# Kernel tuning notes

Hardware: AMD Instinct MI355X
Metric: run time of the kernel (lower is better)

## Reference

```python
import jax, jax.numpy as jnp
import numpy as np

B, T, H, Dk = 2, 2048, 8, 64
D = H * Dk
MAX_TIMESCALE = 10000.0
MIN_TIMESCALE = 2.0


def sinusoid_position_encoding(seq_len, hidden):
    # Non-causal symmetric relative positions: length 2*seq_len.
    freqs = np.arange(0, hidden, MIN_TIMESCALE)
    inv_freq = MAX_TIMESCALE ** (-freqs / hidden)
    pos_seq = np.arange(seq_len, -seq_len, -1.0)  # [2T]
    sinusoid = np.einsum('i,j->ij', pos_seq, inv_freq)  # [2T, hidden/2]
    pe = np.concatenate([np.sin(sinusoid), np.cos(sinusoid)], axis=-1)
    return jnp.asarray(pe, dtype=jnp.float32)  # [2T, hidden]


def rel_shift(logits):
    # Transformer-XL shift (general, non-causal): [b,h,t,2t] -> [b,h,t,t]
    b, h, t, total = logits.shape  # total == 2t
    x = logits.reshape(b, h, total, t)[:, :, 1:, :]
    x = x.reshape(b, h, t, total - 1)
    return x[..., :t]


def setup_inputs() -> dict:
    key = jax.random.key(0)
    ks = jax.random.split(key, 14)
    s = 1.0 / np.sqrt(D).astype(np.float32)  # VarianceScaling(1.0)-like
    return {
        'query': jax.random.normal(ks[0], (B, T, D), jnp.float32),
        'key_in': jax.random.normal(ks[1], (B, T, D), jnp.float32),
        'value': jax.random.normal(ks[2], (B, T, D), jnp.float32),
        'Wq': jax.random.normal(ks[3], (D, H * Dk), jnp.float32) * s,
        'bq': jnp.zeros((H * Dk,), jnp.float32),
        'Wk': jax.random.normal(ks[4], (D, H * Dk), jnp.float32) * s,
        'bk': jnp.zeros((H * Dk,), jnp.float32),
        'Wv': jax.random.normal(ks[5], (D, H * Dk), jnp.float32) * s,
        'bv': jnp.zeros((H * Dk,), jnp.float32),
        'Wr': jax.random.normal(ks[6], (D, D), jnp.float32) * s,
        'content_bias': jax.random.normal(ks[7], (H, Dk), jnp.float32) * 0.02,
        'relative_bias': jax.random.normal(ks[8], (H, Dk), jnp.float32) * 0.02,
        'Wo': jax.random.normal(ks[9], (H * Dk, D), jnp.float32) * s,
        'bo': jnp.zeros((D,), jnp.float32),
    }


def reference(query, key_in, value, Wq, bq, Wk, bk, Wv, bv, Wr,
              content_bias, relative_bias, Wo, bo):
    q = (query @ Wq + bq).reshape(B, T, H, Dk)
    k = (key_in @ Wk + bk).reshape(B, T, H, Dk)
    v = (value @ Wv + bv).reshape(B, T, H, Dk)

    # Content logits with learned per-head content bias.
    content_logits = jnp.einsum('bthd,bThd->bhtT', q + content_bias, k)

    # Relative-position keys: sinusoid encodings projected (no bias).
    pos = sinusoid_position_encoding(T, D)          # [2T, D]
    rel_k = (pos @ Wr).reshape(2 * T, H, Dk)        # [2T, H, Dk]
    relative_logits = jnp.einsum('bthd,Thd->bhtT', q + relative_bias, rel_k)
    relative_logits = rel_shift(relative_logits)    # [B,H,T,T]

    attn_logits = (content_logits + relative_logits) / np.sqrt(Dk).astype(np.float32)
    attn_weights = jax.nn.softmax(attn_logits)      # [B,H,T,T]

    attn = jnp.einsum('bhtT,bThd->bthd', attn_weights, v)
    attn_vec = attn.reshape(B, T, H * Dk)
    return attn_vec @ Wo + bo
```

## Files before the change

kernel.cpp:

```cpp
#include <hip/hip_runtime.h>
#include <math.h>

#define BB 2
#define TT 2048
#define HH 8
#define DK 64
#define DD 512
#define MM (BB * TT)
#define WSZ (128 * 4096)

typedef unsigned int u32;
typedef unsigned short u16;
typedef __bf16 bf16x8 __attribute__((ext_vector_type(8)));
typedef float f32x4 __attribute__((ext_vector_type(4)));

union frag_u { bf16x8 f; u16 u[8]; u32 w[4]; };

__device__ __forceinline__ void split2(float x, u16& h, u16& l) {
    u32 u = __float_as_uint(x);
    u32 hi = (u + 0x7fffu + ((u >> 16) & 1u)) >> 16;
    float hif = __uint_as_float(hi << 16);
    float lof = x - hif;
    u32 ul = __float_as_uint(lof);
    u32 lo = (ul + 0x7fffu + ((ul >> 16) & 1u)) >> 16;
    h = (u16)hi; l = (u16)lo;
}
__device__ __forceinline__ u16 bf16_rne(float x) {
    u32 u = __float_as_uint(x);
    return (u16)((u + 0x7fffu + ((u >> 16) & 1u)) >> 16);
}

__device__ __forceinline__ void load_lds16(const void* g, void* l) {
    __builtin_amdgcn_global_load_lds(
        (const __attribute__((address_space(1))) void*)g,
        (__attribute__((address_space(3))) void*)l, 16, 0, 0);
}

__device__ __forceinline__ void pack_granule(const float* xs, u16* dt, int g) {
    u32 hw[4], lw[4];
#pragma unroll
    for (int e = 0; e < 4; e++) {
        u16 h0, l0, h1, l1;
        split2(xs[2 * e], h0, l0);
        split2(xs[2 * e + 1], h1, l1);
        hw[e] = (u32)h0 | ((u32)h1 << 16);
        lw[e] = (u32)l0 | ((u32)l1 << 16);
    }
    *(uint4*)(dt + g * 8)        = make_uint4(hw[0], hw[1], hw[2], hw[3]);
    *(uint4*)(dt + 2048 + g * 8) = make_uint4(lw[0], lw[1], lw[2], lw[3]);
}

__global__ __launch_bounds__(256) void prepack_wpe_kernel(
    const float* __restrict__ W0, const float* __restrict__ W1,
    const float* __restrict__ W2, const float* __restrict__ W3,
    const float* __restrict__ W4, u16* __restrict__ dstW,
    u16* __restrict__ dstPe) {
    __shared__ float tw[64][36];
    const int tid = threadIdx.x;
    if (blockIdx.x < 640) {
        const int bid = blockIdx.x;
        const int widx = bid >> 7, loc = bid & 127;
        const int nb2 = loc >> 3, kb = loc & 7;
        const float* Wsrc = widx == 0 ? W0 : widx == 1 ? W1 : widx == 2 ? W2
                          : widx == 3 ? W3 : W4;
        const int kl = tid >> 2, gr = tid & 3;
        const float* p = Wsrc + (size_t)(kb * 64 + kl) * 512 + nb2 * 32 + gr * 8;
        float4 a  = *(const float4*)p;
        float4 b4 = *(const float4*)(p + 4);
        *(float4*)&tw[kl][gr * 8]     = a;
        *(float4*)&tw[kl][gr * 8 + 4] = b4;
        __syncthreads();
        const int n5 = tid >> 3, f = tid & 7, s = f >> 2, kq = f & 3;
        float xs[8];
#pragma unroll
        for (int e = 0; e < 8; e++) xs[e] = tw[s * 32 + kq * 8 + e][n5];
        const int n = n5 & 15, nt = n5 >> 4;
        const int g = nt * 128 + n * 8 + ((4 * s + kq + 5 * n) & 7);
        pack_granule(xs, dstW + (size_t)bid * 4096, g);
    } else {
        const int bid = blockIdx.x - 640;
        const int r = tid >> 3, f = tid & 7;
        const int m  = (bid >> 3) * 32 + r;
        const int c0 = (bid & 7) * 64 + f * 8;
        float xs[8];
#pragma unroll
        for (int e = 0; e < 8; e++) {
            int col = c0 + e;
            int j = col & 255;
            double inv_freq = exp((double)(-2 * j) * (9.210340371976184 / 512.0));
            double ang = (double)(TT - m) * inv_freq;
            xs[e] = (col < 256) ? (float)sin(ang) : (float)cos(ang);
        }
        const int s = f >> 2, kq = f & 3, nt = r >> 4, n = r & 15;
        const int g = nt * 128 + n * 8 + ((4 * s + kq + 5 * n) & 7);
        pack_granule(xs, dstPe + (size_t)bid * 4096, g);
    }
}

__device__ __forceinline__ void prepack_a_body(
    const float* __restrict__ src, u16* __restrict__ dst, int bid, int tid) {
    const int r = tid >> 3, f = tid & 7;
    const float* p = src + ((size_t)(bid >> 3) * 32 + r) * 512
                         + (size_t)(bid & 7) * 64 + f * 8;
    float4 a  = *(const float4*)p;
    float4 b4 = *(const float4*)(p + 4);
    float xs[8] = {a.x, a.y, a.z, a.w, b4.x, b4.y, b4.z, b4.w};
    const int s = f >> 2, kq = f & 3, nt = r >> 4, n = r & 15;
    const int g = nt * 128 + n * 8 + ((4 * s + kq + 5 * n) & 7);
    pack_granule(xs, dst + (size_t)bid * 4096, g);
}

__global__ __launch_bounds__(256) void prepack_a3_kernel(
    const float* __restrict__ sq, const float* __restrict__ sk,
    const float* __restrict__ sv, u16* __restrict__ dq,
    u16* __restrict__ dk, u16* __restrict__ dv) {
    const int sel = blockIdx.x >> 10, sub = blockIdx.x & 1023;
    const float* s = sel == 0 ? sq : sel == 1 ? sk : sv;
    u16* d = sel == 0 ? dq : sel == 1 ? dk : dv;
    prepack_a_body(s, d, sub, threadIdx.x);
}

__device__ __forceinline__ void gemm_full(
    const u16* __restrict__ Apk, const u16* __restrict__ Wpk,
    const float* __restrict__ bias, float* __restrict__ C,
    u16* __restrict__ Ppk, const float* __restrict__ dotv,
    float* __restrict__ dotout, int EPI, int bx, int tid) {
    __shared__ __align__(16) u16 Stage[2][16384];

    const int w = tid >> 6, lane = tid & 63, quad = lane >> 4, c = lane & 15;
    const int mp = bx & 63, nb = bx >> 6;
    const int mq = w >> 1, nq = w & 1;

    auto stage_async = [&](int kb, int half) {
        const u16* s = (w < 2)
            ? Apk + (size_t)((2 * mp + w) * 8 + kb) * 4096
            : Wpk + (size_t)((2 * nb + (w & 1)) * 8 + kb) * 4096;
        const u16* g = s + lane * 8;
        u16* d = Stage[half] + w * 4096;
#pragma unroll
        for (int u2 = 0; u2 < 8; u2++)
            load_lds16(g + u2 * 512, d + u2 * 512);
    };

    stage_async(0, 0);

    f32x4 acc[2][2];
#pragma unroll
    for (int mh = 0; mh < 2; mh++)
#pragma unroll
        for (int nh = 0; nh < 2; nh++) acc[mh][nh] = (f32x4){0.f, 0.f, 0.f, 0.f};

    for (int kb = 0; kb < 8; kb++) {
        const int half = kb & 1;
        __syncthreads();
        if (kb < 7) stage_async(kb + 1, 1 - half);
        const u16* Ab = Stage[half] + mq * 4096;
        const u16* Wb = Stage[half] + 8192 + nq * 4096;
#pragma unroll
        for (int s = 0; s < 2; s++) {
            bf16x8 ah[2], al[2], wh[2], wl[2];
#pragma unroll
            for (int t = 0; t < 2; t++) {
                int g = (t << 7) + (c << 3) + (((s << 2) + quad + 5 * c) & 7);
                ah[t] = *(const bf16x8*)(Ab + g * 8);
                al[t] = *(const bf16x8*)(Ab + 2048 + g * 8);
                wh[t] = *(const bf16x8*)(Wb + g * 8);
                wl[t] = *(const bf16x8*)(Wb + 2048 + g * 8);
            }
#pragma unroll
            for (int mh = 0; mh < 2; mh++)
#pragma unroll
                for (int nh = 0; nh < 2; nh++) {
                    acc[mh][nh] = __builtin_amdgcn_mfma_f32_16x16x32_bf16(
                        ah[mh], wh[nh], acc[mh][nh], 0, 0, 0);
                    acc[mh][nh] = __builtin_amdgcn_mfma_f32_16x16x32_bf16(
                        ah[mh], wl[nh], acc[mh][nh], 0, 0, 0);
                    acc[mh][nh] = __builtin_amdgcn_mfma_f32_16x16x32_bf16(
                        al[mh], wh[nh], acc[mh][nh], 0, 0, 0);
                }
        }
    }

    const int n0 = nb * 64 + nq * 32;
    float bv0 = bias ? bias[n0 + c] : 0.f;
    float bv1 = bias ? bias[n0 + 16 + c] : 0.f;

    if (EPI == 0) {
        const int m0 = mp * 64 + mq * 32;
#pragma unroll
        for (int mh = 0; mh < 2; mh++)
#pragma unroll
            for (int r = 0; r < 4; r++) {
                size_t row = (size_t)(m0 + mh * 16 + quad * 4 + r) * 512;
                C[row + n0 + c]      = acc[mh][0][r] + bv0;
                C[row + n0 + 16 + c] = acc[mh][1][r] + bv1;
            }
        return;
    }

    __syncthreads();
    float (*Cl)[68] = (float (*)[68])Stage;
    {
        const int rbase = mq * 32;
#pragma unroll
        for (int mh = 0; mh < 2; mh++)
#pragma unroll
            for (int r = 0; r < 4; r++) {
                int row = rbase + mh * 16 + quad * 4 + r;
                Cl[row][nq * 32 + c]      = acc[mh][0][r] + bv0;
                Cl[row][nq * 32 + 16 + c] = acc[mh][1][r] + bv1;
            }
    }
    __syncthreads();

    if (EPI == 2) {
        const int b = mp >> 5, jt0 = (mp & 31) * 2;
        const int d = tid >> 2, kq = tid & 3;
        const int n = d & 15;
        const int g = (d >> 4) * 64 + n * 4 + ((kq + (n >> 1)) & 3);
#pragma unroll
        for (int ht = 0; ht < 2; ht++) {
            float xs[8];
#pragma unroll
            for (int e = 0; e < 8; e++) xs[e] = Cl[ht * 32 + kq * 8 + e][d];
            u16* dt = Ppk + (size_t)(b * 512 + nb * 64 + jt0 + ht) * 4096;
            pack_granule(xs, dt, g);
        }
        return;
    }

    {
        const int rr = tid >> 3, f = tid & 7;
        const int s = f >> 2, kq = f & 3, nt = rr >> 4, n = rr & 15;
        const int g = nt * 128 + n * 8 + ((4 * s + kq + 5 * n) & 7);
#pragma unroll
        for (int ht = 0; ht < 2; ht++) {
            float xs[8];
#pragma unroll
            for (int e = 0; e < 8; e++) xs[e] = Cl[ht * 32 + rr][f * 8 + e];
            size_t tidx = (EPI == 1)
                ? (size_t)((mp >> 5) * 512 + nb * 64 + (mp & 31) * 2 + ht)
                : (size_t)(nb * 128 + mp * 2 + ht);
            pack_granule(xs, Ppk + tidx * 4096, g);
        }
    }
    if (tid < 64) {
        const float* dv = dotv + nb * 64;
        const float* rowp = Cl[tid];
        float sacc = 0.f;
#pragma unroll
        for (int d = 0; d < 64; d++) sacc += dv[d] * rowp[d];
        int m = mp * 64 + tid;
        if (EPI == 1) {
            int b = m >> 11, t = m & 2047;
            dotout[((size_t)nb * BB + b) * TT + t] = sacc * 0.125f - 8.0f;
        } else {
            dotout[(size_t)nb * 4096 + m] = sacc * 0.125f;
        }
    }
}

__global__ __launch_bounds__(256, 2) void gemm_mfma_kernel(
    const u16* __restrict__ Apk, const u16* __restrict__ Wpk,
    const float* __restrict__ bias, float* __restrict__ C) {
    gemm_full(Apk, Wpk, bias, C, nullptr, nullptr, nullptr, 0,
              blockIdx.x, threadIdx.x);
}

__global__ __launch_bounds__(256, 2) void gemm_relk_kernel(
    const u16* __restrict__ Apk, const u16* __restrict__ Wpk,
    const float* __restrict__ rb, u16* __restrict__ Rpk,
    float* __restrict__ rbrk) {
    gemm_full(Apk, Wpk, nullptr, nullptr, Rpk, rb, rbrk, 3,
              blockIdx.x, threadIdx.x);
}

__global__ __launch_bounds__(256, 2) void gemm3_mfma_kernel(
    const u16* __restrict__ Aq, const u16* __restrict__ Ak,
    const u16* __restrict__ Av, const u16* __restrict__ Wpk,
    const float* __restrict__ bq, const float* __restrict__ bk,
    const float* __restrict__ bv, const float* __restrict__ cb,
    float* __restrict__ qb, u16* __restrict__ Kpk, u16* __restrict__ Vpk,
    float* __restrict__ cbk) {
    const int widx = blockIdx.x >> 9, bx = blockIdx.x & 511;
    const u16* A = widx == 0 ? Aq : widx == 1 ? Ak : Av;
    const u16* W = Wpk + (size_t)widx * WSZ;
    const float* bias = widx == 0 ? bq : widx == 1 ? bk : bv;
    float* Cq = widx == 0 ? qb : nullptr;
    u16* P = widx == 1 ? Kpk : widx == 2 ? Vpk : nullptr;
    gemm_full(A, W, bias, Cq, P, widx == 1 ? cb : nullptr,
              widx == 1 ? cbk : nullptr, widx, bx, threadIdx.x);
}

__global__ __launch_bounds__(128, 2) void attn_mfma_kernel(
    const float* __restrict__ q, const u16* __restrict__ Kpk,
    const u16* __restrict__ Vpk, const u16* __restrict__ Rpk,
    const float* __restrict__ cbk, const float* __restrict__ rbrk,
    u16* __restrict__ Aout) {
    __shared__ float Ring[2 * 3 * 1120];
    __shared__ __align__(16) u16 Pbuf[2 * 1280];

    const int tid = threadIdx.x;
    const int w = tid >> 6, lane = tid & 63, quad = lane >> 4, c = lane & 15;
    const int bx = blockIdx.x;
    const int h = bx & 7, b = (bx >> 3) & 1, it = bx >> 4;
    const int i0 = it * 32;
    const size_t bh_off = (size_t)b * TT * DD + (size_t)h * DK;

    frag_u qh[2][2], ql[2][2];
#pragma unroll
    for (int rg = 0; rg < 2; rg++) {
        const float* qrow = q + bh_off + (size_t)(i0 + 16 * rg + c) * DD;
#pragma unroll
        for (int s = 0; s < 2; s++) {
            int d0 = s * 32 + quad * 8;
            float4 a  = *(const float4*)(qrow + d0);
            float4 b4 = *(const float4*)(qrow + d0 + 4);
            float xs[8] = {a.x, a.y, a.z, a.w, b4.x, b4.y, b4.z, b4.w};
#pragma unroll
            for (int j2 = 0; j2 < 8; j2++)
                split2(xs[j2] * 0.125f, qh[rg][s].u[j2], ql[rg][s].u[j2]);
        }
    }

    frag_u onesf;
#pragma unroll
    for (int j2 = 0; j2 < 8; j2++) onesf.u[j2] = 0x3f80u;

    const u16* Ktiles  = Kpk + (size_t)(b * HH + h) * 64 * 4096;
    const u16* Vtiles  = Vpk + (size_t)(b * HH + h) * 64 * 4096;
    const u16* Rchunks = Rpk + (size_t)h * 128 * 4096;
    const float* rbrk_h = rbrk + (size_t)h * (2 * TT);
    const float* cbk_h  = cbk + ((size_t)h * BB + b) * TT;

    auto read_kr = [&](const u16* reg, int nt, int s, bf16x8& fh, bf16x8& fl) {
        int g = (nt << 7) + (c << 3) + (((s << 2) + quad + 5 * c) & 7);
        fh = *(const bf16x8*)(reg + g * 8);
        fl = *(const bf16x8*)(reg + 2048 + g * 8);
    };
    auto read_v = [&](const u16* Vb, int ntd, bf16x8& fh, bf16x8& fl) {
        int g = ntd * 64 + c * 4 + ((quad + (c >> 1)) & 3);
        fh = *(const bf16x8*)(Vb + g * 8);
        fl = *(const bf16x8*)(Vb + 2048 + g * 8);
    };

    auto produce = [&](int cidx) {
        const u16* Rc = Rchunks + (size_t)cidx * 4096;
        float* ringw = Ring + (w * 3 + cidx % 3) * 1120;
#pragma unroll
        for (int ntp = 0; ntp < 2; ntp++) {
            f32x4 a0 = {0.f, 0.f, 0.f, 0.f};
            f32x4 a1 = {0.f, 0.f, 0.f, 0.f};
#pragma unroll
            for (int s = 0; s < 2; s++) {
                int g = (ntp << 7) + (c << 3) + (((s << 2) + quad + 5 * c) & 7);
                bf16x8 fh = *(const bf16x8*)(Rc + g * 8);
                bf16x8 fl = *(const bf16x8*)(Rc + 2048 + g * 8);
                a0 = __builtin_amdgcn_mfma_f32_16x16x32_bf16(qh[0][s].f, fh, a0, 0, 0, 0);
                a0 = __builtin_amdgcn_mfma_f32_16x16x32_bf16(qh[0][s].f, fl, a0, 0, 0, 0);
                a0 = __builtin_amdgcn_mfma_f32_16x16x32_bf16(ql[0][s].f, fh, a0, 0, 0, 0);
                a1 = __builtin_amdgcn_mfma_f32_16x16x32_bf16(qh[1][s].f, fh, a1, 0, 0, 0);
                a1 = __builtin_amdgcn_mfma_f32_16x16x32_bf16(qh[1][s].f, fl, a1, 0, 0, 0);
                a1 = __builtin_amdgcn_mfma_f32_16x16x32_bf16(ql[1][s].f, fh, a1, 0, 0, 0);
            }
            float rbv = rbrk_h[cidx * 32 + ntp * 16 + c];
            int mpos = ntp * 16 + c;
#pragma unroll
            for (int r = 0; r < 4; r++)
                ringw[(quad * 4 + r) * 35 + mpos] = a0[r] + rbv;
#pragma unroll
            for (int r = 0; r < 4; r++)
                ringw[(16 + quad * 4 + r) * 35 + mpos] = a1[r] + rbv;
        }
    };

    const int base = TT - i0 + 1024 * w;
    const int F = (base >> 5) - 1;
    produce(F);
    produce(F + 1);

    f32x4 o[2][4];
    f32x4 acc_l[2];
#pragma unroll
    for (int rg = 0; rg < 2; rg++) {
        acc_l[rg] = (f32x4){0.f, 0.f, 0.f, 0.f};
#pragma unroll
        for (int nt = 0; nt < 4; nt++) o[rg][nt] = (f32x4){0.f, 0.f, 0.f, 0.f};
    }

    for (int t = 0; t < 32; t++) {
        const int j0 = 1024 * w + 32 * t;
        const u16* Kb = Ktiles + (size_t)(w * 32 + t) * 4096;
        const u16* Vb = Vtiles + (size_t)(w * 32 + t) * 4096;

        int cnext = F + t + 2;
        if (cnext < 128) produce(cnext);

        const int slo = (F + t) % 3;
        const int shi = (slo == 2) ? 0 : slo + 1;
        const int off_lo = (w * 3 + slo) * 1120;
        const int off_hi = (w * 3 + shi) * 1120;
        float cbv0 = cbk_h[j0 + c];
        float cbv1 = cbk_h[j0 + 16 + c];
        float sv[2][2][4];
#pragma unroll
        for (int nt = 0; nt < 2; nt++) {
            f32x4 sc0 = {0.f, 0.f, 0.f, 0.f};
            f32x4 sc1 = {0.f, 0.f, 0.f, 0.f};
            bf16x8 fh0, fl0, fh1, fl1;
            read_kr(Kb, nt, 0, fh0, fl0);
            read_kr(Kb, nt, 1, fh1, fl1);
            __builtin_amdgcn_s_setprio(1);
            sc0 = __builtin_amdgcn_mfma_f32_16x16x32_bf16(qh[0][0].f, fh0, sc0, 0, 0, 0);
            sc0 = __builtin_amdgcn_mfma_f32_16x16x32_bf16(qh[0][0].f, fl0, sc0, 0, 0, 0);
            sc0 = __builtin_amdgcn_mfma_f32_16x16x32_bf16(ql[0][0].f, fh0, sc0, 0, 0, 0);
            sc0 = __builtin_amdgcn_mfma_f32_16x16x32_bf16(qh[0][1].f, fh1, sc0, 0, 0, 0);
            sc0 = __builtin_amdgcn_mfma_f32_16x16x32_bf16(qh[0][1].f, fl1, sc0, 0, 0, 0);
            sc0 = __builtin_amdgcn_mfma_f32_16x16x32_bf16(ql[0][1].f, fh1, sc0, 0, 0, 0);
            sc1 = __builtin_amdgcn_mfma_f32_16x16x32_bf16(qh[1][0].f, fh0, sc1, 0, 0, 0);
            sc1 = __builtin_amdgcn_mfma_f32_16x16x32_bf16(qh[1][0].f, fl0, sc1, 0, 0, 0);
            sc1 = __builtin_amdgcn_mfma_f32_16x16x32_bf16(ql[1][0].f, fh0, sc1, 0, 0, 0);
            sc1 = __builtin_amdgcn_mfma_f32_16x16x32_bf16(qh[1][1].f, fh1, sc1, 0, 0, 0);
            sc1 = __builtin_amdgcn_mfma_f32_16x16x32_bf16(qh[1][1].f, fl1, sc1, 0, 0, 0);
            sc1 = __builtin_amdgcn_mfma_f32_16x16x32_bf16(ql[1][1].f, fh1, sc1, 0, 0, 0);
            __builtin_amdgcn_s_setprio(0);
            float cbv = nt ? cbv1 : cbv0;
#pragma unroll
            for (int r = 0; r < 4; r++) {
                int row16 = quad * 4 + r;
                int rel0 = nt * 16 + c - row16 + 32;
                float rv0 = Ring[((rel0 >= 32) ? off_hi : off_lo)
                                 + row16 * 35 + (rel0 & 31)];
                sv[0][nt][r] = sc0[r] + rv0 + cbv;
                int rel1 = rel0 - 16;
                float rv1 = Ring[((rel1 >= 32) ? off_hi : off_lo)
                                 + (16 + row16) * 35 + (rel1 & 31)];
                sv[1][nt][r] = sc1[r] + rv1 + cbv;
            }
        }

#pragma unroll
        for (int rg = 0; rg < 2; rg++)
#pragma unroll
            for (int r = 0; r < 4; r++) {
                u16* pb = Pbuf + w * 1280 + (16 * rg + quad * 4 + r) * 40;
                pb[c]      = bf16_rne(__expf(sv[rg][0][r]));
                pb[16 + c] = bf16_rne(__expf(sv[rg][1][r]));
            }

        frag_u ph[2];
#pragma unroll
        for (int rg = 0; rg < 2; rg++) {
            const u16* pb = Pbuf + w * 1280 + (16 * rg + c) * 40 + quad * 8;
            *(uint4*)&ph[rg] = *(const uint4*)pb;
        }
        __builtin_amdgcn_s_setprio(1);
#pragma unroll
        for (int ntd = 0; ntd < 4; ntd++) {
            bf16x8 vh, vl;
            read_v(Vb, ntd, vh, vl);
            o[0][ntd] = __builtin_amdgcn_mfma_f32_16x16x32_bf16(ph[0].f, vh, o[0][ntd], 0, 0, 0);
            o[0][ntd] = __builtin_amdgcn_mfma_f32_16x16x32_bf16(ph[0].f, vl, o[0][ntd], 0, 0, 0);
            o[1][ntd] = __builtin_amdgcn_mfma_f32_16x16x32_bf16(ph[1].f, vh, o[1][ntd], 0, 0, 0);
            o[1][ntd] = __builtin_amdgcn_mfma_f32_16x16x32_bf16(ph[1].f, vl, o[1][ntd], 0, 0, 0);
        }
        acc_l[0] = __builtin_amdgcn_mfma_f32_16x16x32_bf16(ph[0].f, onesf.f, acc_l[0], 0, 0, 0);
        acc_l[1] = __builtin_amdgcn_mfma_f32_16x16x32_bf16(ph[1].f, onesf.f, acc_l[1], 0, 0, 0);
        __builtin_amdgcn_s_setprio(0);
    }

    float* scr = Ring + 3360;
    if (w == 1) {
#pragma unroll
        for (int rg = 0; rg < 2; rg++) {
#pragma unroll
            for (int nt = 0; nt < 4; nt++)
#pragma unroll
                for (int r = 0; r < 4; r++)
                    scr[(16 * rg + quad * 4 + r) * 65 + nt * 16 + c] = o[rg][nt][r];
            if (c == 0) {
#pragma unroll
                for (int r = 0; r < 4; r++)
                    scr[2080 + 16 * rg + quad * 4 + r] = acc_l[rg][r];
            }
        }
    }
    __syncthreads();
    float* Lp = Ring;
    if (w == 0) {
#pragma unroll
        for (int rg = 0; rg < 2; rg++)
#pragma unroll
            for (int r = 0; r < 4; r++) {
                int row16 = quad * 4 + r;
                int row32 = 16 * rg + row16;
                float invl = 1.0f / (acc_l[rg][r] + scr[2080 + row32]);
#pragma unroll
                for (int nt = 0; nt < 4; nt++)
                    Lp[row32 * 68 + nt * 16 + c] =
                        (o[rg][nt][r] + scr[row32 * 65 + nt * 16 + c]) * invl;
            }
    }
    __syncthreads();
    u16* dt = Aout + (size_t)((b * 64 + it) * 8 + h) * 4096;
#pragma unroll
    for (int pass = 0; pass < 2; pass++) {
        int idx = pass * 128 + tid;
        int rr = idx >> 3, f = idx & 7;
        float xs[8];
#pragma unroll
        for (int e = 0; e < 8; e++) xs[e] = Lp[rr * 68 + f * 8 + e];
        int s = f >> 2, kq = f & 3, nt2 = rr >> 4, n = rr & 15;
        int g = nt2 * 128 + n * 8 + ((4 * s + kq + 5 * n) & 7);
        pack_granule(xs, dt, g);
    }
}

extern "C" void kernel_launch(void* const* d_in, const int* in_sizes, int n_in,
                              void* d_out, int out_size, void* d_ws, size_t ws_size,
                              hipStream_t stream) {
    const float* query  = (const float*)d_in[0];
    const float* key_in = (const float*)d_in[1];
    const float* value  = (const float*)d_in[2];
    const float* Wq = (const float*)d_in[3];
    const float* bq = (const float*)d_in[4];
    const float* Wk = (const float*)d_in[5];
    const float* bk = (const float*)d_in[6];
    const float* Wv = (const float*)d_in[7];
    const float* bv = (const float*)d_in[8];
    const float* Wr = (const float*)d_in[9];
    const float* cb = (const float*)d_in[10];
    const float* rb = (const float*)d_in[11];
    const float* Wo = (const float*)d_in[12];
    const float* bo = (const float*)d_in[13];
    float* out = (float*)d_out;

    float* ws = (float*)d_ws;
    const size_t SL = (size_t)MM * DD;
    float* qb   = ws;
    u16*   Kpk  = (u16*)(ws + 1 * SL);
    u16*   Vpk  = (u16*)(ws + 2 * SL);
    u16*   Rpk  = (u16*)(ws + 3 * SL);
    u16*   s4   = (u16*)(ws + 4 * SL);
    u16*   s5   = (u16*)(ws + 5 * SL);
    u16*   s6   = (u16*)(ws + 6 * SL);
    u16*   Wpk  = (u16*)(ws + 7 * SL);
    float* cbk  = ws + 7 * SL + 1310720;
    float* rbrk = cbk + BB * TT * HH;

    prepack_wpe_kernel<<<1664, 256, 0, stream>>>(Wq, Wk, Wv, Wr, Wo, Wpk, s6);

    gemm_relk_kernel<<<512, 256, 0, stream>>>(s6, Wpk + 3 * WSZ, rb, Rpk, rbrk);

    prepack_a3_kernel<<<3072, 256, 0, stream>>>(query, key_in, value,
                                                s6, s5, s4);
    gemm3_mfma_kernel<<<1536, 256, 0, stream>>>(s6, s5, s4, Wpk, bq, bk, bv,
                                                cb, qb, Kpk, Vpk, cbk);

    attn_mfma_kernel<<<BB * HH * (TT / 32), 128, 0, stream>>>(
        qb, Kpk, Vpk, Rpk, cbk, rbrk, s4);

    gemm_mfma_kernel<<<512, 256, 0, stream>>>(s4, Wpk + 4 * WSZ, bo, out);
}
```

Measured before the change: 250.5 us.

## Software-pipeline K fragment loads and hoist R/V loads in attention loop

Restructures the attention inner loop into a two-stage unrolled body that double-buffers K fragments in registers, loading the next tile's K while the current tile's QK MFMAs run. R-chunk and V fragments are issued as global loads at the top of each iteration, and the relative-logit ring production is moved after the score computation so that memory latency overlaps with MFMA work. This adds substantial register pressure, which risks lower occupancy or spills.

After: 399.6 us. 1.6x slower.

```diff
diff --git a/kernel.cpp b/kernel.cpp
--- a/kernel.cpp
+++ b/kernel.cpp
@@ -376,6 +376,18 @@
 
     const int base = TT - i0 + 1024 * w;
     const int F = (base >> 5) - 1;
+
+    bf16x8 KAh[2][2], KAl[2][2], KBh[2][2], KBl[2][2];
+    auto load_Kfr = [&](int tile, bf16x8 (&fh)[2][2], bf16x8 (&fl)[2][2]) {
+        const u16* Kb = Ktiles + (size_t)tile * 4096;
+#pragma unroll
+        for (int nt = 0; nt < 2; nt++)
+#pragma unroll
+            for (int s = 0; s < 2; s++)
+                read_kr(Kb, nt, s, fh[nt][s], fl[nt][s]);
+    };
+
+    load_Kfr(w * 32, KAh, KAl);
     produce(F);
     produce(F + 1);
 
@@ -388,42 +400,60 @@
         for (int nt = 0; nt < 4; nt++) o[rg][nt] = (f32x4){0.f, 0.f, 0.f, 0.f};
     }
 
-    for (int t = 0; t < 32; t++) {
+    auto body = [&](int t, bf16x8 (&ckh)[2][2], bf16x8 (&ckl)[2][2],
+                    bf16x8 (&nkh)[2][2], bf16x8 (&nkl)[2][2]) {
         const int j0 = 1024 * w + 32 * t;
-        const u16* Kb = Ktiles + (size_t)(w * 32 + t) * 4096;
-        const u16* Vb = Vtiles + (size_t)(w * 32 + t) * 4096;
-
-        int cnext = F + t + 2;
-        if (cnext < 128) produce(cnext);
+        const int cnext = F + t + 2;
+
+        bf16x8 rfh[2][2], rfl[2][2];
+        if (cnext < 128) {
+            const u16* Rc = Rchunks + (size_t)cnext * 4096;
+#pragma unroll
+            for (int ntp = 0; ntp < 2; ntp++)
+#pragma unroll
+                for (int s = 0; s < 2; s++) {
+                    int g = (ntp << 7) + (c << 3) + (((s << 2) + quad + 5 * c) & 7);
+                    rfh[ntp][s] = *(const bf16x8*)(Rc + g * 8);
+                    rfl[ntp][s] = *(const bf16x8*)(Rc + 2048 + g * 8);
+                }
+        }
+        bf16x8 vfh[4], vfl[4];
+        {
+            const u16* Vb = Vtiles + (size_t)(w * 32 + t) * 4096;
+#pragma unroll
+            for (int ntd = 0; ntd < 4; ntd++) read_v(Vb, ntd, vfh[ntd], vfl[ntd]);
+        }
+        float cbv0 = cbk_h[j0 + c];
+        float cbv1 = cbk_h[j0 + 16 + c];
+
+        f32x4 sc0[2], sc1[2];
+        __builtin_amdgcn_s_setprio(1);
+#pragma unroll
+        for (int nt = 0; nt < 2; nt++) {
+            f32x4 a0 = {0.f, 0.f, 0.f, 0.f};
+            f32x4 a1 = {0.f, 0.f, 0.f, 0.f};
+#pragma unroll
+            for (int s = 0; s < 2; s++) {
+                a0 = __builtin_amdgcn_mfma_f32_16x16x32_bf16(qh[0][s].f, ckh[nt][s], a0, 0, 0, 0);
+                a0 = __builtin_amdgcn_mfma_f32_16x16x32_bf16(qh[0][s].f, ckl[nt][s], a0, 0, 0, 0);
+                a0 = __builtin_amdgcn_mfma_f32_16x16x32_bf16(ql[0][s].f, ckh[nt][s], a0, 0, 0, 0);
+                a1 = __builtin_amdgcn_mfma_f32_16x16x32_bf16(qh[1][s].f, ckh[nt][s], a1, 0, 0, 0);
+                a1 = __builtin_amdgcn_mfma_f32_16x16x32_bf16(qh[1][s].f, ckl[nt][s], a1, 0, 0, 0);
+                a1 = __builtin_amdgcn_mfma_f32_16x16x32_bf16(ql[1][s].f, ckh[nt][s], a1, 0, 0, 0);
+            }
+            sc0[nt] = a0; sc1[nt] = a1;
+        }
+        __builtin_amdgcn_s_setprio(0);
+
+        if (t < 31) load_Kfr(w * 32 + t + 1, nkh, nkl);
 
         const int slo = (F + t) % 3;
         const int shi = (slo == 2) ? 0 : slo + 1;
         const int off_lo = (w * 3 + slo) * 1120;
         const int off_hi = (w * 3 + shi) * 1120;
-        float cbv0 = cbk_h[j0 + c];
-        float cbv1 = cbk_h[j0 + 16 + c];
         float sv[2][2][4];
 #pragma unroll
         for (int nt = 0; nt < 2; nt++) {
-            f32x4 sc0 = {0.f, 0.f, 0.f, 0.f};
-            f32x4 sc1 = {0.f, 0.f, 0.f, 0.f};
-            bf16x8 fh0, fl0, fh1, fl1;
-            read_kr(Kb, nt, 0, fh0, fl0);
-            read_kr(Kb, nt, 1, fh1, fl1);
-            __builtin_amdgcn_s_setprio(1);
-            sc0 = __builtin_amdgcn_mfma_f32_16x16x32_bf16(qh[0][0].f, fh0, sc0, 0, 0, 0);
-            sc0 = __builtin_amdgcn_mfma_f32_16x16x32_bf16(qh[0][0].f, fl0, sc0, 0, 0, 0);
-            sc0 = __builtin_amdgcn_mfma_f32_16x16x32_bf16(ql[0][0].f, fh0, sc0, 0, 0, 0);
-            sc0 = __builtin_amdgcn_mfma_f32_16x16x32_bf16(qh[0][1].f, fh1, sc0, 0, 0, 0);
-            sc0 = __builtin_amdgcn_mfma_f32_16x16x32_bf16(qh[0][1].f, fl1, sc0, 0, 0, 0);
-            sc0 = __builtin_amdgcn_mfma_f32_16x16x32_bf16(ql[0][1].f, fh1, sc0, 0, 0, 0);
-            sc1 = __builtin_amdgcn_mfma_f32_16x16x32_bf16(qh[1][0].f, fh0, sc1, 0, 0, 0);
-            sc1 = __builtin_amdgcn_mfma_f32_16x16x32_bf16(qh[1][0].f, fl0, sc1, 0, 0, 0);
-            sc1 = __builtin_amdgcn_mfma_f32_16x16x32_bf16(ql[1][0].f, fh0, sc1, 0, 0, 0);
-            sc1 = __builtin_amdgcn_mfma_f32_16x16x32_bf16(qh[1][1].f, fh1, sc1, 0, 0, 0);
-            sc1 = __builtin_amdgcn_mfma_f32_16x16x32_bf16(qh[1][1].f, fl1, sc1, 0, 0, 0);
-            sc1 = __builtin_amdgcn_mfma_f32_16x16x32_bf16(ql[1][1].f, fh1, sc1, 0, 0, 0);
-            __builtin_amdgcn_s_setprio(0);
             float cbv = nt ? cbv1 : cbv0;
 #pragma unroll
             for (int r = 0; r < 4; r++) {
@@ -431,12 +461,40 @@
                 int rel0 = nt * 16 + c - row16 + 32;
                 float rv0 = Ring[((rel0 >= 32) ? off_hi : off_lo)
                                  + row16 * 35 + (rel0 & 31)];
-                sv[0][nt][r] = sc0[r] + rv0 + cbv;
+                sv[0][nt][r] = sc0[nt][r] + rv0 + cbv;
                 int rel1 = rel0 - 16;
                 float rv1 = Ring[((rel1 >= 32) ? off_hi : off_lo)
                                  + (16 + row16) * 35 + (rel1 & 31)];
-                sv[1][nt][r] = sc1[r] + rv1 + cbv;
-            }
+                sv[1][nt][r] = sc1[nt][r] + rv1 + cbv;
+            }
+        }
+
+        if (cnext < 128) {
+            float* ringw = Ring + (w * 3 + cnext % 3) * 1120;
+            __builtin_amdgcn_s_setprio(1);
+#pragma unroll
+            for (int ntp = 0; ntp < 2; ntp++) {
+                f32x4 a0 = {0.f, 0.f, 0.f, 0.f};
+                f32x4 a1 = {0.f, 0.f, 0.f, 0.f};
+#pragma unroll
+                for (int s = 0; s < 2; s++) {
+                    a0 = __builtin_amdgcn_mfma_f32_16x16x32_bf16(qh[0][s].f, rfh[ntp][s], a0, 0, 0, 0);
+                    a0 = __builtin_amdgcn_mfma_f32_16x16x32_bf16(qh[0][s].f, rfl[ntp][s], a0, 0, 0, 0);
+                    a0 = __builtin_amdgcn_mfma_f32_16x16x32_bf16(ql[0][s].f, rfh[ntp][s], a0, 0, 0, 0);
+                    a1 = __builtin_amdgcn_mfma_f32_16x16x32_bf16(qh[1][s].f, rfh[ntp][s], a1, 0, 0, 0);
+                    a1 = __builtin_amdgcn_mfma_f32_16x16x32_bf16(qh[1][s].f, rfl[ntp][s], a1, 0, 0, 0);
+                    a1 = __builtin_amdgcn_mfma_f32_16x16x32_bf16(ql[1][s].f, rfh[ntp][s], a1, 0, 0, 0);
+                }
+                float rbv = rbrk_h[cnext * 32 + ntp * 16 + c];
+                int mpos = ntp * 16 + c;
+#pragma unroll
+                for (int r = 0; r < 4; r++)
+                    ringw[(quad * 4 + r) * 35 + mpos] = a0[r] + rbv;
+#pragma unroll
+                for (int r = 0; r < 4; r++)
+                    ringw[(16 + quad * 4 + r) * 35 + mpos] = a1[r] + rbv;
+            }
+            __builtin_amdgcn_s_setprio(0);
         }
 
 #pragma unroll
@@ -447,26 +505,29 @@
                 pb[c]      = bf16_rne(__expf(sv[rg][0][r]));
                 pb[16 + c] = bf16_rne(__expf(sv[rg][1][r]));
             }
-
         frag_u ph[2];
 #pragma unroll
         for (int rg = 0; rg < 2; rg++) {
             const u16* pb = Pbuf + w * 1280 + (16 * rg + c) * 40 + quad * 8;
             *(uint4*)&ph[rg] = *(const uint4*)pb;
         }
+
         __builtin_amdgcn_s_setprio(1);
 #pragma unroll
         for (int ntd = 0; ntd < 4; ntd++) {
-            bf16x8 vh, vl;
-            read_v(Vb, ntd, vh, vl);
-            o[0][ntd] = __builtin_amdgcn_mfma_f32_16x16x32_bf16(ph[0].f, vh, o[0][ntd], 0, 0, 0);
-            o[0][ntd] = __builtin_amdgcn_mfma_f32_16x16x32_bf16(ph[0].f, vl, o[0][ntd], 0, 0, 0);
-            o[1][ntd] = __builtin_amdgcn_mfma_f32_16x16x32_bf16(ph[1].f, vh, o[1][ntd], 0, 0, 0);
-            o[1][ntd] = __builtin_amdgcn_mfma_f32_16x16x32_bf16(ph[1].f, vl, o[1][ntd], 0, 0, 0);
+            o[0][ntd] = __builtin_amdgcn_mfma_f32_16x16x32_bf16(ph[0].f, vfh[ntd], o[0][ntd], 0, 0, 0);
+            o[0][ntd] = __builtin_amdgcn_mfma_f32_16x16x32_bf16(ph[0].f, vfl[ntd], o[0][ntd], 0, 0, 0);
+            o[1][ntd] = __builtin_amdgcn_mfma_f32_16x16x32_bf16(ph[1].f, vfh[ntd], o[1][ntd], 0, 0, 0);
+            o[1][ntd] = __builtin_amdgcn_mfma_f32_16x16x32_bf16(ph[1].f, vfl[ntd], o[1][ntd], 0, 0, 0);
         }
         acc_l[0] = __builtin_amdgcn_mfma_f32_16x16x32_bf16(ph[0].f, onesf.f, acc_l[0], 0, 0, 0);
         acc_l[1] = __builtin_amdgcn_mfma_f32_16x16x32_bf16(ph[1].f, onesf.f, acc_l[1], 0, 0, 0);
         __builtin_amdgcn_s_setprio(0);
+    };
+
+    for (int t2 = 0; t2 < 32; t2 += 2) {
+        body(t2,     KAh, KAl, KBh, KBl);
+        body(t2 + 1, KBh, KBl, KAh, KAl);
     }
 
     float* scr = Ring + 3360;
```
